# Kernel tuning notes

Hardware: AMD Instinct MI355X
Metric: run time of the kernel (lower is better)

The kernel has to match this reference:

```python
import jax, jax.numpy as jnp
import numpy as np

N, E, IN_C, OUT_C, HEADS = 50000, 800000, 256, 256, 4
C = OUT_C // HEADS  # per-head channels = 64
BN_EPS = 1e-5


def setup_inputs() -> dict:
    key = jax.random.key(0)
    ks = jax.random.split(key, 16)
    inp = {
        'x': jax.random.normal(ks[0], (N, IN_C), dtype=jnp.float32),
        'edge_index': jax.random.randint(ks[1], (2, E), 0, N, dtype=jnp.int64),
        'edge_attr': jax.random.uniform(ks[2], (E, 1), dtype=jnp.float32),
        'spatial_coords': jax.random.normal(ks[3], (N, 2), dtype=jnp.float32),
        # GATConv params
        'W_gat': jax.random.normal(ks[4], (IN_C, HEADS * C), dtype=jnp.float32) * 0.05,
        'att_src': jax.random.normal(ks[5], (HEADS, C), dtype=jnp.float32) * 0.05,
        'att_dst': jax.random.normal(ks[6], (HEADS, C), dtype=jnp.float32) * 0.05,
        'bias_gat': jnp.zeros((HEADS * C,), dtype=jnp.float32),
        # spatial_attention MLP (computed but unused by the original forward)
        'w1': jax.random.normal(ks[7], (1, 64), dtype=jnp.float32) * 0.05,
        'b1': jnp.zeros((64,), dtype=jnp.float32),
        'w2': jax.random.normal(ks[8], (64, HEADS), dtype=jnp.float32) * 0.05,
        'b2': jnp.zeros((HEADS,), dtype=jnp.float32),
        # feature_transform: Linear + BatchNorm1d (eval stats) + ReLU (+Dropout=identity)
        'w_ft': jax.random.normal(ks[9], (IN_C, OUT_C), dtype=jnp.float32) * 0.05,
        'b_ft': jnp.zeros((OUT_C,), dtype=jnp.float32),
        'bn_gamma': jnp.ones((OUT_C,), dtype=jnp.float32),
        'bn_beta': jnp.zeros((OUT_C,), dtype=jnp.float32),
        'bn_mean': jax.random.normal(ks[10], (OUT_C,), dtype=jnp.float32) * 0.01,
        'bn_var': jax.random.uniform(ks[11], (OUT_C,), dtype=jnp.float32, minval=0.5, maxval=1.5),
    }
    return inp


def _forward(x, edge_index, edge_attr, W_gat, att_src, att_dst, bias_gat,
             w1, b1, w2, b2, w_ft, b_ft, bn_gamma, bn_beta, bn_mean, bn_var):
    n = x.shape[0]
    # add self-loops (PyG GATConv default)
    loop = jnp.arange(n, dtype=edge_index.dtype)
    src = jnp.concatenate([edge_index[0], loop])
    dst = jnp.concatenate([edge_index[1], loop])

    # linear transform: [N, heads, C]
    h = (x @ W_gat).reshape(n, HEADS, C)
    a_src = jnp.einsum('nhc,hc->nh', h, att_src)  # [N, H]
    a_dst = jnp.einsum('nhc,hc->nh', h, att_dst)  # [N, H]

    # per-edge attention logits, LeakyReLU(0.2)
    alpha = jax.nn.leaky_relu(a_src[src] + a_dst[dst], negative_slope=0.2)  # [Etot, H]
    # segment softmax over incoming edges of each destination node
    amax = jax.ops.segment_max(alpha, dst, num_segments=n)
    alpha = jnp.exp(alpha - amax[dst])
    denom = jax.ops.segment_sum(alpha, dst, num_segments=n)
    alpha = alpha / (denom[dst] + 1e-16)

    # weighted message aggregation
    msg = h[src] * alpha[:, :, None]                        # [Etot, H, C]
    agg = jax.ops.segment_sum(msg, dst, num_segments=n)     # [N, H, C]
    gat_out = agg.reshape(n, HEADS * C) + bias_gat

    # spatial attention weights (computed but UNUSED, matching original)
    spatial_weights = jax.nn.sigmoid(jax.nn.relu(edge_attr @ w1 + b1) @ w2 + b2)
    del spatial_weights

    # feature_transform (BatchNorm in eval mode, Dropout identity)
    y = x @ w_ft + b_ft
    y = (y - bn_mean) * jax.lax.rsqrt(bn_var + BN_EPS) * bn_gamma + bn_beta
    transformed = jax.nn.relu(y)

    return gat_out + transformed


def reference(x, edge_index, edge_attr, spatial_coords, W_gat, att_src, att_dst,
              bias_gat, w1, b1, w2, b2, w_ft, b_ft, bn_gamma, bn_beta, bn_mean, bn_var):
    # spatial_coords is accepted but unused by the original module's forward
    return _forward(x, edge_index, edge_attr, W_gat, att_src, att_dst, bias_gat,
                    w1, b1, w2, b2, w_ft, b_ft, bn_gamma, bn_beta, bn_mean, bn_var)
```

## Files before the change

### kernel.cpp

```cpp
#include <hip/hip_runtime.h>
#include <math.h>

typedef __attribute__((ext_vector_type(4))) float  f32x4;
typedef __attribute__((ext_vector_type(8))) short  short8;
typedef __attribute__((ext_vector_type(8))) unsigned short usx8;

__device__ __forceinline__ unsigned short f2bf(float f) {
    union { float f; unsigned int i; } c; c.f = f;
    unsigned int x = c.i;
    unsigned int r = (x + 0x7FFFu + ((x >> 16) & 1u)) >> 16;
    return (unsigned short)r;
}

__global__ __launch_bounds__(256) void k_prep(
    int* __restrict__ zr, int zn,
    const float* __restrict__ Wg, const float* __restrict__ Wf,
    unsigned short* __restrict__ wbt,
    const float* __restrict__ x, unsigned short* __restrict__ xb,
    long total8, int nz) {
    int b = blockIdx.x;
    if (b < nz) {
        int i = b * 256 + threadIdx.x;
        if (i < zn) zr[i] = 0;
        return;
    }
    b -= nz;
    if (b < 512) {
        int idx = b * 256 + threadIdx.x;
        int c = idx >> 8;
        int k = idx & 255;
        float v = (c < 256) ? Wg[k * 256 + c] : Wf[k * 256 + (c - 256)];
        wbt[idx] = f2bf(v);
        return;
    }
    b -= 512;
    long i = (long)b * 256 + threadIdx.x;
    if (i >= total8 || !xb) return;
    const f32x4* p = (const f32x4*)x;
    f32x4 v0 = p[2 * i], v1 = p[2 * i + 1];
    usx8 o;
    o[0] = f2bf(v0[0]); o[1] = f2bf(v0[1]); o[2] = f2bf(v0[2]); o[3] = f2bf(v0[3]);
    o[4] = f2bf(v1[0]); o[5] = f2bf(v1[1]); o[6] = f2bf(v1[2]); o[7] = f2bf(v1[3]);
    ((usx8*)xb)[i] = o;
}

#define BM 128
#define BN 128

__global__ __launch_bounds__(256, 4) void k_gemm_fast(
    const unsigned short* __restrict__ xb,
    const unsigned short* __restrict__ wbt,
    unsigned short* __restrict__ hb,
    unsigned short* __restrict__ tb,
    float* __restrict__ out,
    const float* __restrict__ att_s, const float* __restrict__ att_d,
    float* __restrict__ a_src, float* __restrict__ a_dst,
    const float* __restrict__ b_ft, const float* __restrict__ bn_g,
    const float* __restrict__ bn_b, const float* __restrict__ bn_m,
    const float* __restrict__ bn_v, int M) {
    __shared__ unsigned short As[128 * 64];
    __shared__ unsigned short Bs[128 * 64];
    const int t = threadIdx.x;
    const int w = t >> 6, l = t & 63;
    const int wr = w >> 1, wc = w & 1;
    const int bm0 = blockIdx.y * BM;
    const int bn0 = blockIdx.x * BN;
    const int kg = l >> 4;
    const int lm = l & 15;

    const int srow = l >> 3;
    const int scol = ((l & 7) ^ srow) << 3;

    f32x4 acc[4][4] = {};

    for (int kk = 0; kk < 4; kk++) {
        const int k0 = kk * 64;
        __syncthreads();
#pragma unroll
        for (int j = 0; j < 4; j++) {
            int r = ((w * 4 + j) << 3) + srow;
            int ga = bm0 + r; if (ga >= M) ga = M - 1;
            __builtin_amdgcn_global_load_lds(
                (const __attribute__((address_space(1))) unsigned int*)
                    (xb + (long)ga * 256 + k0 + scol),
                (__attribute__((address_space(3))) unsigned int*)
                    (As + ((w * 4 + j) << 9)),
                16, 0, 0);
            __builtin_amdgcn_global_load_lds(
                (const __attribute__((address_space(1))) unsigned int*)
                    (wbt + (long)(bn0 + r) * 256 + k0 + scol),
                (__attribute__((address_space(3))) unsigned int*)
                    (Bs + ((w * 4 + j) << 9)),
                16, 0, 0);
        }
        __syncthreads();
#pragma unroll
        for (int ks = 0; ks < 2; ks++) {
            const int cb = (ks * 64 + kg * 16) ^ ((lm & 7) << 4);
            short8 afr[4], bfr[4];
#pragma unroll
            for (int mi = 0; mi < 4; mi++) {
                int row = wr * 64 + mi * 16 + lm;
                afr[mi] = *(const short8*)((const char*)As + row * 128 + cb);
            }
#pragma unroll
            for (int nj = 0; nj < 4; nj++) {
                int row = wc * 64 + nj * 16 + lm;
                bfr[nj] = *(const short8*)((const char*)Bs + row * 128 + cb);
            }
#pragma unroll
            for (int mi = 0; mi < 4; mi++)
#pragma unroll
                for (int nj = 0; nj < 4; nj++)
                    acc[mi][nj] = __builtin_amdgcn_mfma_f32_16x16x32_bf16(
                        afr[mi], bfr[nj], acc[mi][nj], 0, 0, 0);
        }
    }

    const bool isH = (bn0 < 256);
#pragma unroll
    for (int mi = 0; mi < 4; mi++) {
#pragma unroll
        for (int nj = 0; nj < 4; nj++) {
            int col = bn0 + wc * 64 + nj * 16 + lm;
            f32x4 a = acc[mi][nj];
            int rowbase = bm0 + wr * 64 + mi * 16 + kg * 4;
            if (isH) {
#pragma unroll
                for (int r = 0; r < 4; r++) {
                    int row = rowbase + r;
                    if (row < M) hb[(long)row * 256 + col] = f2bf(a[r]);
                }
            } else {
                int c2 = col - 256;
                float bft = b_ft[c2], mu = bn_m[c2];
                float iv = rsqrtf(bn_v[c2] + 1e-5f);
                float g = bn_g[c2], bt = bn_b[c2];
#pragma unroll
                for (int r = 0; r < 4; r++) {
                    int row = rowbase + r;
                    if (row < M) {
                        float v = (a[r] + bft - mu) * iv * g + bt;
                        v = v > 0.f ? v : 0.f;
                        if (tb) tb[(long)row * 256 + c2] = f2bf(v);
                        else    out[(long)row * 256 + c2] = v;
                    }
                }
            }
        }
    }

    if (isH) {
        const int head = (bn0 >> 6) + wc;
        float as_c[4], ad_c[4];
#pragma unroll
        for (int nj = 0; nj < 4; nj++) {
            as_c[nj] = att_s[head * 64 + nj * 16 + lm];
            ad_c[nj] = att_d[head * 64 + nj * 16 + lm];
        }
#pragma unroll
        for (int mi = 0; mi < 4; mi++) {
#pragma unroll
            for (int r = 0; r < 4; r++) {
                float s1 = 0.f, s2 = 0.f;
#pragma unroll
                for (int nj = 0; nj < 4; nj++) {
                    s1 = fmaf(acc[mi][nj][r], as_c[nj], s1);
                    s2 = fmaf(acc[mi][nj][r], ad_c[nj], s2);
                }
#pragma unroll
                for (int o = 1; o < 16; o <<= 1) {
                    s1 += __shfl_xor(s1, o);
                    s2 += __shfl_xor(s2, o);
                }
                int row = bm0 + wr * 64 + mi * 16 + kg * 4 + r;
                if (lm == 0 && row < M) {
                    a_src[(long)row * 4 + head] = s1;
                    a_dst[(long)row * 4 + head] = s2;
                }
            }
        }
    }
}

#define BK 32
__global__ __launch_bounds__(256) void k_gemm(
    const float* __restrict__ x, const unsigned short* __restrict__ wbt,
    unsigned short* __restrict__ hb, unsigned short* __restrict__ tb,
    float* __restrict__ out,
    const float* __restrict__ att_s, const float* __restrict__ att_d,
    float* __restrict__ a_src, float* __restrict__ a_dst,
    const float* __restrict__ b_ft, const float* __restrict__ bn_g,
    const float* __restrict__ bn_b, const float* __restrict__ bn_m,
    const float* __restrict__ bn_v, int M) {
    __shared__ unsigned short As[BM][BK + 8];
    __shared__ unsigned short Bs[BN][BK + 8];
    const int t = threadIdx.x;
    const int w = t >> 6, lane = t & 63;
    const int wr = w >> 1, wc = w & 1;
    const int bm0 = blockIdx.y * BM;
    const int bn0 = blockIdx.x * BN;
    const int kg = lane >> 4;
    const int lm = lane & 15;
    f32x4 acc[4][4] = {};
    for (int k0 = 0; k0 < 256; k0 += BK) {
        f32x4 a0[2], a1[2];
        usx8 bv[2];
#pragma unroll
        for (int s = 0; s < 2; s++) {
            int seg = t + s * 256;
            int row = seg >> 2;
            int off = (seg & 3) * 8;
            int grow = bm0 + row; if (grow >= M) grow = M - 1;
            const float* ap = x + (long)grow * 256 + k0 + off;
            a0[s] = *(const f32x4*)ap;
            a1[s] = *(const f32x4*)(ap + 4);
            bv[s] = *(const usx8*)(wbt + (long)(bn0 + row) * 256 + k0 + off);
        }
        __syncthreads();
#pragma unroll
        for (int s = 0; s < 2; s++) {
            int seg = t + s * 256;
            int row = seg >> 2;
            int off = (seg & 3) * 8;
            usx8 av;
            av[0] = f2bf(a0[s][0]); av[1] = f2bf(a0[s][1]);
            av[2] = f2bf(a0[s][2]); av[3] = f2bf(a0[s][3]);
            av[4] = f2bf(a1[s][0]); av[5] = f2bf(a1[s][1]);
            av[6] = f2bf(a1[s][2]); av[7] = f2bf(a1[s][3]);
            *(usx8*)&As[row][off] = av;
            *(usx8*)&Bs[row][off] = bv[s];
        }
        __syncthreads();
        short8 afr[4], bfr[4];
#pragma unroll
        for (int mi = 0; mi < 4; mi++)
            afr[mi] = *(const short8*)&As[wr * 64 + mi * 16 + lm][kg * 8];
#pragma unroll
        for (int nj = 0; nj < 4; nj++)
            bfr[nj] = *(const short8*)&Bs[wc * 64 + nj * 16 + lm][kg * 8];
#pragma unroll
        for (int mi = 0; mi < 4; mi++)
#pragma unroll
            for (int nj = 0; nj < 4; nj++)
                acc[mi][nj] = __builtin_amdgcn_mfma_f32_16x16x32_bf16(
                    afr[mi], bfr[nj], acc[mi][nj], 0, 0, 0);
        __syncthreads();
    }
    const bool isH = (bn0 < 256);
#pragma unroll
    for (int mi = 0; mi < 4; mi++) {
#pragma unroll
        for (int nj = 0; nj < 4; nj++) {
            int col = bn0 + wc * 64 + nj * 16 + lm;
            f32x4 a = acc[mi][nj];
            int rowbase = bm0 + wr * 64 + mi * 16 + kg * 4;
            if (isH) {
#pragma unroll
                for (int r = 0; r < 4; r++) {
                    int row = rowbase + r;
                    if (row < M) hb[(long)row * 256 + col] = f2bf(a[r]);
                }
            } else {
                int c2 = col - 256;
                float bft = b_ft[c2], mu = bn_m[c2];
                float iv = rsqrtf(bn_v[c2] + 1e-5f);
                float g = bn_g[c2], bt = bn_b[c2];
#pragma unroll
                for (int r = 0; r < 4; r++) {
                    int row = rowbase + r;
                    if (row < M) {
                        float v = (a[r] + bft - mu) * iv * g + bt;
                        v = v > 0.f ? v : 0.f;
                        if (tb) tb[(long)row * 256 + c2] = f2bf(v);
                        else    out[(long)row * 256 + c2] = v;
                    }
                }
            }
        }
    }
    if (isH) {
        const int head = (bn0 >> 6) + wc;
        float as_c[4], ad_c[4];
#pragma unroll
        for (int nj = 0; nj < 4; nj++) {
            as_c[nj] = att_s[head * 64 + nj * 16 + lm];
            ad_c[nj] = att_d[head * 64 + nj * 16 + lm];
        }
#pragma unroll
        for (int mi = 0; mi < 4; mi++) {
#pragma unroll
            for (int r = 0; r < 4; r++) {
                float s1 = 0.f, s2 = 0.f;
#pragma unroll
                for (int nj = 0; nj < 4; nj++) {
                    s1 = fmaf(acc[mi][nj][r], as_c[nj], s1);
                    s2 = fmaf(acc[mi][nj][r], ad_c[nj], s2);
                }
#pragma unroll
                for (int o = 1; o < 16; o <<= 1) {
                    s1 += __shfl_xor(s1, o);
                    s2 += __shfl_xor(s2, o);
                }
                int row = bm0 + wr * 64 + mi * 16 + kg * 4 + r;
                if (lm == 0 && row < M) {
                    a_src[(long)row * 4 + head] = s1;
                    a_dst[(long)row * 4 + head] = s2;
                }
            }
        }
    }
}

__global__ void k_count(const int* __restrict__ ei, int* __restrict__ deg, int E) {
    int i = blockIdx.x * blockDim.x + threadIdx.x;
    if (i < E) atomicAdd(&deg[ei[E + i]], 1);
}
__global__ __launch_bounds__(256) void k_scan1(const int* __restrict__ deg,
                                               int* __restrict__ offs,
                                               int* __restrict__ bsum, int n) {
    __shared__ int tmp[256];
    int b = blockIdx.x, t = threadIdx.x;
    int base = b * 1024;
    int v[4];
#pragma unroll
    for (int j = 0; j < 4; j++) {
        int i = base + t * 4 + j;
        v[j] = (i < n) ? (deg[i] + 1) : 0;
    }
    int local = v[0] + v[1] + v[2] + v[3];
    tmp[t] = local;
    __syncthreads();
    for (int off = 1; off < 256; off <<= 1) {
        int xv = (t >= off) ? tmp[t - off] : 0;
        __syncthreads();
        tmp[t] += xv;
        __syncthreads();
    }
    int run = tmp[t] - local;
    if (t == 255) bsum[b] = tmp[255];
#pragma unroll
    for (int j = 0; j < 4; j++) {
        int i = base + t * 4 + j;
        if (i < n) offs[i] = run;
        run += v[j];
    }
}
__global__ void k_scan3f(int* __restrict__ offs, const int* __restrict__ bsum,
                         int* __restrict__ srcs, int n) {
    int i = blockIdx.x * blockDim.x + threadIdx.x;
    if (i >= n) return;
    int nbi = i >> 10;
    int s = 0;
    for (int j = 0; j < nbi; j++) s += bsum[j];
    int o = offs[i] + s;
    offs[i] = o;
    srcs[o] = i;
}
__global__ void k_scatter(const int* __restrict__ ei, const int* __restrict__ offs,
                          int* __restrict__ cursor, int* __restrict__ srcs, int E) {
    int i = blockIdx.x * blockDim.x + threadIdx.x;
    if (i >= E) return;
    int d = ei[E + i];
    int pos = atomicAdd(&cursor[d], 1);
    srcs[offs[d] + 1 + pos] = ei[i];
}

__global__ __launch_bounds__(256, 4) void k_agg(
    const int* __restrict__ offs, const int* __restrict__ srcs,
    const unsigned short* __restrict__ hb,
    const float* __restrict__ a_src, const float* __restrict__ a_dst,
    const float* __restrict__ bias_gat, const unsigned short* __restrict__ tb,
    float* __restrict__ out, int N, int E) {
    const int n = (blockIdx.x * 256 + threadIdx.x) >> 6;
    const int l = threadIdx.x & 63;
    if (n >= N) return;
    const int head = l >> 4;
    const int sub = l & 15;
    const int beg = offs[n];
    const int end = (n + 1 < N) ? offs[n + 1] : (E + N);
    const uint2* hp = (const uint2*)hb + l;

    const float ad = a_dst[(long)n * 4 + head];
    f32x4 acc = {};
    float den = 0.f;

    for (int base = beg; base < end; base += 16) {
        const int len = min(16, end - base);
        int sv = 0;
        float wsel = 0.f;
        if (base + sub < end) {
            sv = srcs[base + sub];
            float lv = a_src[(long)sv * 4 + head] + ad;
            lv = fmaxf(lv, 0.2f * lv);
            wsel = __expf(lv);
        }

        if (len == 16) {
            uint2 hv[16];
#pragma unroll
            for (int i = 0; i < 16; ++i) {
                int src = __shfl(sv, i);
                const uint2* ap = hp + ((long)src << 6);
                asm volatile("global_load_dwordx2 %0, %1, off"
                             : "=v"(hv[i]) : "v"(ap));
            }
            float wg[16];
#pragma unroll
            for (int i = 0; i < 16; ++i) wg[i] = __shfl(wsel, (l & 48) + i);
            asm volatile("s_waitcnt vmcnt(0)" ::: "memory");
            __builtin_amdgcn_sched_barrier(0);
#pragma unroll
            for (int i = 0; i < 16; ++i) {
                den += wg[i];
                acc[0] = fmaf(wg[i], __uint_as_float(hv[i].x << 16), acc[0]);
                acc[1] = fmaf(wg[i], __uint_as_float(hv[i].x & 0xFFFF0000u), acc[1]);
                acc[2] = fmaf(wg[i], __uint_as_float(hv[i].y << 16), acc[2]);
                acc[3] = fmaf(wg[i], __uint_as_float(hv[i].y & 0xFFFF0000u), acc[3]);
            }
        } else {
            for (int i = 0; i < len; ++i) {
                int src = __shfl(sv, i);
                float wgt = __shfl(wsel, (l & 48) + i);
                uint2 hv = hp[(long)src << 6];
                den += wgt;
                acc[0] = fmaf(wgt, __uint_as_float(hv.x << 16), acc[0]);
                acc[1] = fmaf(wgt, __uint_as_float(hv.x & 0xFFFF0000u), acc[1]);
                acc[2] = fmaf(wgt, __uint_as_float(hv.y << 16), acc[2]);
                acc[3] = fmaf(wgt, __uint_as_float(hv.y & 0xFFFF0000u), acc[3]);
            }
        }
    }

    const float inv = 1.f / (den + 1e-16f);
    const float4 bv = ((const float4*)bias_gat)[l];
    float4 trf;
    const long rowoff = ((long)n << 8) + l * 4;
    if (tb) {
        uint2 tv = ((const uint2*)(tb + ((long)n << 8)))[l];
        trf.x = __uint_as_float(tv.x << 16);
        trf.y = __uint_as_float(tv.x & 0xFFFF0000u);
        trf.z = __uint_as_float(tv.y << 16);
        trf.w = __uint_as_float(tv.y & 0xFFFF0000u);
    } else {
        trf = *(const float4*)(out + rowoff);
    }
    float4 r;
    r.x = acc[0] * inv + bv.x + trf.x;
    r.y = acc[1] * inv + bv.y + trf.y;
    r.z = acc[2] * inv + bv.z + trf.z;
    r.w = acc[3] * inv + bv.w + trf.w;
    *(float4*)(out + rowoff) = r;
}

extern "C" void kernel_launch(void* const* d_in, const int* in_sizes, int n_in,
                              void* d_out, int out_size, void* d_ws, size_t ws_size,
                              hipStream_t stream) {
    const float* x        = (const float*)d_in[0];
    const int*   ei       = (const int*)d_in[1];
    const float* W_gat    = (const float*)d_in[4];
    const float* att_src  = (const float*)d_in[5];
    const float* att_dst  = (const float*)d_in[6];
    const float* bias_gat = (const float*)d_in[7];
    const float* w_ft     = (const float*)d_in[12];
    const float* b_ft     = (const float*)d_in[13];
    const float* bn_g     = (const float*)d_in[14];
    const float* bn_b     = (const float*)d_in[15];
    const float* bn_m     = (const float*)d_in[16];
    const float* bn_v     = (const float*)d_in[17];
    float* out = (float*)d_out;

    const int N = in_sizes[0] / 256;
    const int E = in_sizes[1] / 2;
    const int ETOT = E + N;

    char* p = (char*)d_ws;
    char* pend = p + ws_size;
    auto alloc = [&](size_t bytes) {
        void* r = (void*)p;
        p += (bytes + 255) & ~(size_t)255;
        return r;
    };
    unsigned short* wbt  = (unsigned short*)alloc((size_t)512 * 256 * 2);
    unsigned short* hb   = (unsigned short*)alloc((size_t)N * 256 * 2);
    float* a_src = (float*)alloc((size_t)N * 4 * 4);
    float* a_dst = (float*)alloc((size_t)N * 4 * 4);
    char* z0 = p;
    int* deg    = (int*)alloc((size_t)N * 4);
    int* cursor = (int*)alloc((size_t)N * 4);
    char* z1 = p;
    int* offs   = (int*)alloc((size_t)(N + 1) * 4);
    int* bsum   = (int*)alloc((size_t)256 * 4);
    int* srcs   = (int*)alloc((size_t)ETOT * 4);
    unsigned short* xb = (unsigned short*)alloc((size_t)N * 256 * 2);
    if (p > pend) xb = nullptr;
    unsigned short* tb = (unsigned short*)alloc((size_t)N * 256 * 2);
    if (p > pend) tb = nullptr;

    const int zn = (int)((z1 - z0) / 4);
    const int nz = (zn + 255) / 256;
    const long total8 = (long)N * 256 / 8;
    const int nx = xb ? (int)((total8 + 255) / 256) : 0;
    k_prep<<<nz + 512 + nx, 256, 0, stream>>>((int*)z0, zn, W_gat, w_ft, wbt,
                                              x, xb, total8, nz);

    dim3 gg(4, (N + BM - 1) / BM);
    if (xb) {
        k_gemm_fast<<<gg, 256, 0, stream>>>(xb, wbt, hb, tb, out, att_src, att_dst,
                                            a_src, a_dst, b_ft, bn_g, bn_b, bn_m, bn_v, N);
    } else {
        k_gemm<<<gg, 256, 0, stream>>>(x, wbt, hb, tb, out, att_src, att_dst,
                                       a_src, a_dst, b_ft, bn_g, bn_b, bn_m, bn_v, N);
    }

    k_count<<<(E + 255) / 256, 256, 0, stream>>>(ei, deg, E);
    int nb = (N + 1023) / 1024;
    k_scan1<<<nb, 256, 0, stream>>>(deg, offs, bsum, N);
    k_scan3f<<<(N + 255) / 256, 256, 0, stream>>>(offs, bsum, srcs, N);
    k_scatter<<<(E + 255) / 256, 256, 0, stream>>>(ei, offs, cursor, srcs, E);

    k_agg<<<(N * 64 + 255) / 256, 256, 0, stream>>>(offs, srcs, hb, a_src, a_dst,
                                                    bias_gat, tb, out, N, E);
}
```

Baseline: 224.8 us.

## Fuse degree counting into x-cast kernel and block scan into GEMM launch

The single prep kernel is split in two. The weight transpose and zeroing run first. A second kernel converts x to bf16 and also does the edge-degree atomic counting, removing the standalone count launch. The first-level prefix scan now runs as extra blocks appended to the GEMM grid, which is flattened to 1D, so it overlaps GEMM work instead of being its own launch. This cuts two kernel launches and lets small graph-preprocessing work fill idle compute units, at the cost of an extra kernel split for the prep stage.

```diff
diff --git a/kernel.cpp b/kernel.cpp
--- a/kernel.cpp
+++ b/kernel.cpp
@@ -12,12 +12,10 @@
     return (unsigned short)r;
 }
 
-__global__ __launch_bounds__(256) void k_prep(
+__global__ __launch_bounds__(256) void k_prep1(
     int* __restrict__ zr, int zn,
     const float* __restrict__ Wg, const float* __restrict__ Wf,
-    unsigned short* __restrict__ wbt,
-    const float* __restrict__ x, unsigned short* __restrict__ xb,
-    long total8, int nz) {
+    unsigned short* __restrict__ wbt, int nz) {
     int b = blockIdx.x;
     if (b < nz) {
         int i = b * 256 + threadIdx.x;
@@ -25,29 +23,36 @@
         return;
     }
     b -= nz;
-    if (b < 512) {
-        int idx = b * 256 + threadIdx.x;
-        int c = idx >> 8;
-        int k = idx & 255;
-        float v = (c < 256) ? Wg[k * 256 + c] : Wf[k * 256 + (c - 256)];
-        wbt[idx] = f2bf(v);
+    int idx = b * 256 + threadIdx.x;
+    int c = idx >> 8;
+    int k = idx & 255;
+    float v = (c < 256) ? Wg[k * 256 + c] : Wf[k * 256 + (c - 256)];
+    wbt[idx] = f2bf(v);
+}
+
+__global__ __launch_bounds__(256) void k_prep2(
+    const float* __restrict__ x, unsigned short* __restrict__ xb, long total8, int nx,
+    const int* __restrict__ ei, int* __restrict__ deg, int E) {
+    int b = blockIdx.x;
+    if (b < nx) {
+        long i = (long)b * 256 + threadIdx.x;
+        if (i >= total8) return;
+        const f32x4* p = (const f32x4*)x;
+        f32x4 v0 = p[2 * i], v1 = p[2 * i + 1];
+        usx8 o;
+        o[0] = f2bf(v0[0]); o[1] = f2bf(v0[1]); o[2] = f2bf(v0[2]); o[3] = f2bf(v0[3]);
+        o[4] = f2bf(v1[0]); o[5] = f2bf(v1[1]); o[6] = f2bf(v1[2]); o[7] = f2bf(v1[3]);
+        ((usx8*)xb)[i] = o;
         return;
     }
-    b -= 512;
-    long i = (long)b * 256 + threadIdx.x;
-    if (i >= total8 || !xb) return;
-    const f32x4* p = (const f32x4*)x;
-    f32x4 v0 = p[2 * i], v1 = p[2 * i + 1];
-    usx8 o;
-    o[0] = f2bf(v0[0]); o[1] = f2bf(v0[1]); o[2] = f2bf(v0[2]); o[3] = f2bf(v0[3]);
-    o[4] = f2bf(v1[0]); o[5] = f2bf(v1[1]); o[6] = f2bf(v1[2]); o[7] = f2bf(v1[3]);
-    ((usx8*)xb)[i] = o;
+    int i = (b - nx) * 256 + threadIdx.x;
+    if (i < E) atomicAdd(&deg[ei[E + i]], 1);
 }
 
 #define BM 128
 #define BN 128
 
-__global__ __launch_bounds__(256, 4) void k_gemm_fast(
+__global__ __launch_bounds__(256, 4) void k_gemm_scan(
     const unsigned short* __restrict__ xb,
     const unsigned short* __restrict__ wbt,
     unsigned short* __restrict__ hb,
@@ -57,14 +62,46 @@
     float* __restrict__ a_src, float* __restrict__ a_dst,
     const float* __restrict__ b_ft, const float* __restrict__ bn_g,
     const float* __restrict__ bn_b, const float* __restrict__ bn_m,
-    const float* __restrict__ bn_v, int M) {
+    const float* __restrict__ bn_v, int M, int ngemm,
+    const int* __restrict__ deg, int* __restrict__ offs, int* __restrict__ bsum) {
     __shared__ unsigned short As[128 * 64];
     __shared__ unsigned short Bs[128 * 64];
+    __shared__ int tmp[256];
+
+    if (blockIdx.x >= ngemm) {
+        int b = blockIdx.x - ngemm, t = threadIdx.x;
+        int base = b * 1024;
+        int v[4];
+#pragma unroll
+        for (int j = 0; j < 4; j++) {
+            int i = base + t * 4 + j;
+            v[j] = (i < M) ? (deg[i] + 1) : 0;
+        }
+        int local = v[0] + v[1] + v[2] + v[3];
+        tmp[t] = local;
+        __syncthreads();
+        for (int off = 1; off < 256; off <<= 1) {
+            int xv = (t >= off) ? tmp[t - off] : 0;
+            __syncthreads();
+            tmp[t] += xv;
+            __syncthreads();
+        }
+        int run = tmp[t] - local;
+        if (t == 255) bsum[b] = tmp[255];
+#pragma unroll
+        for (int j = 0; j < 4; j++) {
+            int i = base + t * 4 + j;
+            if (i < M) offs[i] = run;
+            run += v[j];
+        }
+        return;
+    }
+
     const int t = threadIdx.x;
     const int w = t >> 6, l = t & 63;
     const int wr = w >> 1, wc = w & 1;
-    const int bm0 = blockIdx.y * BM;
-    const int bn0 = blockIdx.x * BN;
+    const int bm0 = (blockIdx.x >> 2) * BM;
+    const int bn0 = (blockIdx.x & 3) * BN;
     const int kg = l >> 4;
     const int lm = l & 15;
 
@@ -312,10 +349,6 @@
     }
 }
 
-__global__ void k_count(const int* __restrict__ ei, int* __restrict__ deg, int E) {
-    int i = blockIdx.x * blockDim.x + threadIdx.x;
-    if (i < E) atomicAdd(&deg[ei[E + i]], 1);
-}
 __global__ __launch_bounds__(256) void k_scan1(const int* __restrict__ deg,
                                                int* __restrict__ offs,
                                                int* __restrict__ bsum, int n) {
@@ -346,6 +379,7 @@
         run += v[j];
     }
 }
+
 __global__ void k_scan3f(int* __restrict__ offs, const int* __restrict__ bsum,
                          int* __restrict__ srcs, int n) {
     int i = blockIdx.x * blockDim.x + threadIdx.x;
@@ -501,23 +535,27 @@
     const int nz = (zn + 255) / 256;
     const long total8 = (long)N * 256 / 8;
     const int nx = xb ? (int)((total8 + 255) / 256) : 0;
-    k_prep<<<nz + 512 + nx, 256, 0, stream>>>((int*)z0, zn, W_gat, w_ft, wbt,
-                                              x, xb, total8, nz);
-
-    dim3 gg(4, (N + BM - 1) / BM);
+    const int ce = (E + 255) / 256;
+    const int nb = (N + 1023) / 1024;
+    const int ngemm = 4 * ((N + BM - 1) / BM);
+
+    k_prep1<<<nz + 512, 256, 0, stream>>>((int*)z0, zn, W_gat, w_ft, wbt, nz);
+
     if (xb) {
-        k_gemm_fast<<<gg, 256, 0, stream>>>(xb, wbt, hb, tb, out, att_src, att_dst,
-                                            a_src, a_dst, b_ft, bn_g, bn_b, bn_m, bn_v, N);
+        k_prep2<<<nx + ce, 256, 0, stream>>>(x, xb, total8, nx, ei, deg, E);
+        k_gemm_scan<<<ngemm + nb, 256, 0, stream>>>(
+            xb, wbt, hb, tb, out, att_src, att_dst, a_src, a_dst,
+            b_ft, bn_g, bn_b, bn_m, bn_v, N, ngemm, deg, offs, bsum);
     } else {
+        k_prep2<<<ce, 256, 0, stream>>>(x, nullptr, 0, 0, ei, deg, E);
+        dim3 gg(4, (N + BM - 1) / BM);
         k_gemm<<<gg, 256, 0, stream>>>(x, wbt, hb, tb, out, att_src, att_dst,
                                        a_src, a_dst, b_ft, bn_g, bn_b, bn_m, bn_v, N);
-    }
-
-    k_count<<<(E + 255) / 256, 256, 0, stream>>>(ei, deg, E);
-    int nb = (N + 1023) / 1024;
-    k_scan1<<<nb, 256, 0, stream>>>(deg, offs, bsum, N);
+        k_scan1<<<nb, 256, 0, stream>>>(deg, offs, bsum, N);
+    }
+
     k_scan3f<<<(N + 255) / 256, 256, 0, stream>>>(offs, bsum, srcs, N);
-    k_scatter<<<(E + 255) / 256, 256, 0, stream>>>(ei, offs, cursor, srcs, E);
+    k_scatter<<<ce, 256, 0, stream>>>(ei, offs, cursor, srcs, E);
 
     k_agg<<<(N * 64 + 255) / 256, 256, 0, stream>>>(offs, srcs, hb, a_src, a_dst,
                                                     bias_gat, tb, out, N, E);
```

Result: faster. 220.2 us, median of 2 (-2.0%).
